# Kernel optimization log

Hardware: AMD Instinct MI355X
Metric: run time of the kernel (lower is better)

Reference implementation:

```python
import jax, jax.numpy as jnp
import numpy as np

H = 24
HEAD_DIM = 128
EPS = 1e-6
IP_SCALE = 1.0

def _rms(x, w):
    return x * jax.lax.rsqrt(jnp.mean(x * x, axis=-1, keepdims=True) + EPS) * w

def _heads(x, B):
    # (B, S, H*D) -> (B, H, S, D)
    return x.reshape(B, x.shape[1], H, HEAD_DIM).transpose(0, 2, 1, 3)

def _merge(x):
    B, h, S, d = x.shape
    return x.transpose(0, 2, 1, 3).reshape(B, S, h * d)

def _sdpa(q, k, v):
    s = jnp.einsum('bhqd,bhkd->bhqk', q, k) * (1.0 / np.sqrt(HEAD_DIM))
    return jnp.einsum('bhqk,bhkd->bhqd', jax.nn.softmax(s, axis=-1), v)

def _rope(x, cos, sin):
    # Flux-style real rotary: interleaved pairs, out = x*cos + rot(x)*sin
    xr = x.reshape(x.shape[:-1] + (-1, 2))
    x1, x2 = xr[..., 0], xr[..., 1]
    xrot = jnp.stack([-x2, x1], axis=-1).reshape(x.shape)
    return x * cos + xrot * sin

def setup_inputs():
    key = jax.random.key(0)
    ks = jax.random.split(key, 24)
    B, S_img, L_txt, D, IP_DIM, N_IP = 1, 2048, 512, 3072, 2048, 1024
    S = S_img + L_txt
    def w(k, i, o):
        return jax.random.normal(k, (i, o), jnp.float32) * 0.02
    def b(k, o):
        return jax.random.normal(k, (o,), jnp.float32) * 0.01
    pos = jnp.arange(S, dtype=jnp.float32)
    freqs = 1.0 / (10000.0 ** (jnp.arange(0, HEAD_DIM, 2, dtype=jnp.float32) / HEAD_DIM))
    ang = pos[:, None] * freqs[None, :]
    cos = jnp.repeat(jnp.cos(ang), 2, axis=-1)  # (S, HEAD_DIM)
    sin = jnp.repeat(jnp.sin(ang), 2, axis=-1)
    return {
        'hidden_states': jax.random.normal(ks[0], (B, S_img, D), jnp.float32),
        'encoder_hidden_states': jax.random.normal(ks[1], (B, L_txt, D), jnp.float32),
        'ip_hidden_states': jax.random.normal(ks[2], (B, N_IP, IP_DIM), jnp.float32),
        'rot_cos': cos, 'rot_sin': sin,
        'Wq': w(ks[3], D, D), 'bq': b(ks[4], D),
        'Wk': w(ks[5], D, D), 'bk': b(ks[6], D),
        'Wv': w(ks[7], D, D), 'bv': b(ks[8], D),
        'norm_q_w': jnp.ones((HEAD_DIM,), jnp.float32),
        'norm_k_w': jnp.ones((HEAD_DIM,), jnp.float32),
        'aWq': w(ks[9], D, D), 'abq': b(ks[10], D),
        'aWk': w(ks[11], D, D), 'abk': b(ks[12], D),
        'aWv': w(ks[13], D, D), 'abv': b(ks[14], D),
        'norm_aq_w': jnp.ones((HEAD_DIM,), jnp.float32),
        'norm_ak_w': jnp.ones((HEAD_DIM,), jnp.float32),
        'Wk_ip': w(ks[15], IP_DIM, D), 'bk_ip': b(ks[16], D),
        'Wv_ip': w(ks[17], IP_DIM, D), 'bv_ip': b(ks[18], D),
        'norm_ipq_w': jnp.ones((HEAD_DIM,), jnp.float32),
        'norm_ipk_w': jnp.ones((HEAD_DIM,), jnp.float32),
        'Wo': w(ks[19], D, D), 'bo': b(ks[20], D),
        'Wao': w(ks[21], D, D), 'bao': b(ks[22], D),
    }

def reference(hidden_states, encoder_hidden_states, ip_hidden_states, rot_cos, rot_sin,
              Wq, bq, Wk, bk, Wv, bv, norm_q_w, norm_k_w,
              aWq, abq, aWk, abk, aWv, abv, norm_aq_w, norm_ak_w,
              Wk_ip, bk_ip, Wv_ip, bv_ip, norm_ipq_w, norm_ipk_w,
              Wo, bo, Wao, bao):
    B, S_img, D = hidden_states.shape
    L = encoder_hidden_states.shape[1]
    q = _heads(hidden_states @ Wq + bq, B)   # (B,H,S_img,d)
    k = _heads(hidden_states @ Wk + bk, B)
    v = _heads(hidden_states @ Wv + bv, B)
    # IP-adapter cross-attention: RMS-normed raw image query vs projected image tokens
    ip_q = _rms(q, norm_ipq_w)
    ip_k = _rms(_heads(ip_hidden_states @ Wk_ip + bk_ip, B), norm_ipk_w)
    ip_v = _heads(ip_hidden_states @ Wv_ip + bv_ip, B)
    ip_out = _merge(_sdpa(ip_q, ip_k, ip_v))  # (B, S_img, D)
    # main joint attention with per-head QK RMSNorm
    q = _rms(q, norm_q_w)
    k = _rms(k, norm_k_w)
    eq = _rms(_heads(encoder_hidden_states @ aWq + abq, B), norm_aq_w)
    ek = _rms(_heads(encoder_hidden_states @ aWk + abk, B), norm_ak_w)
    ev = _heads(encoder_hidden_states @ aWv + abv, B)
    q = jnp.concatenate([eq, q], axis=2)
    k = jnp.concatenate([ek, k], axis=2)
    v = jnp.concatenate([ev, v], axis=2)
    q = _rope(q, rot_cos, rot_sin)
    k = _rope(k, rot_cos, rot_sin)
    hs = _merge(_sdpa(q, k, v))  # (B, L+S_img, D)
    enc = hs[:, :L]
    img = hs[:, L:] + IP_SCALE * ip_out
    img = img @ Wo + bo
    enc = enc @ Wao + bao
    return (img, enc)
```

## Files before the change

kernel.cpp:

```cpp
#include <hip/hip_runtime.h>
#include <hip/hip_bf16.h>
#include <cmath>
#include <cstdint>

#define H_    24
#define HD_   128
#define D_    3072
#define SIMG_ 2048
#define LTXT_ 512
#define SALL_ 2560
#define NIP_  1024
#define IPD_  2048

using bf16 = __hip_bfloat16;
typedef __bf16 bf16x8 __attribute__((ext_vector_type(8)));
typedef float  f32x4  __attribute__((ext_vector_type(4)));
typedef short  short8 __attribute__((ext_vector_type(8)));

#define QSCALE_ 0.12751741f

#define SWZ_BLOCK(bx, by)                                              \
  {                                                                    \
    int _gx = gridDim.x;                                               \
    int _hw = blockIdx.x + blockIdx.y * _gx;                           \
    int _n  = _gx * gridDim.y;                                         \
    int _lid = (_hw & 7) * (_n >> 3) + (_hw >> 3);                     \
    bx = _lid % _gx;                                                   \
    by = _lid / _gx;                                                   \
  }

__device__ __forceinline__ unsigned short f2bf(float f) {
  unsigned int u = __float_as_uint(f);
  unsigned int r = (u + 0x7fffu + ((u >> 16) & 1u)) >> 16;
  return (unsigned short)r;
}
__device__ __forceinline__ float bf2f(unsigned short u) {
  return __uint_as_float(((unsigned int)u) << 16);
}

__device__ __forceinline__ void gload16(const void* g, void* l) {
  __builtin_amdgcn_global_load_lds(
      (const __attribute__((address_space(1))) unsigned*)g,
      (__attribute__((address_space(3))) unsigned*)l, 16, 0, 0);
}

__global__ void cast_kernel(const float* __restrict__ x, unsigned short* __restrict__ y, int n4) {
  int i = blockIdx.x * blockDim.x + threadIdx.x;
  if (i >= n4) return;
  float4 v = reinterpret_cast<const float4*>(x)[i];
  ushort4 o = make_ushort4(f2bf(v.x), f2bf(v.y), f2bf(v.z), f2bf(v.w));
  reinterpret_cast<ushort4*>(y)[i] = o;
}

__global__ __launch_bounds__(512)
void transpose_cast3_kernel(const float* __restrict__ W0, const float* __restrict__ W1,
                            const float* __restrict__ W2, unsigned short* __restrict__ Wt,
                            int R, int C) {
  __shared__ float tile[32][69];
  const float* W = blockIdx.z == 0 ? W0 : (blockIdx.z == 1 ? W1 : W2);
  unsigned short* dst = Wt + (size_t)blockIdx.z * R * C;
  int bx = blockIdx.x * 64, by = blockIdx.y * 32;
  int tx = threadIdx.x, ty = threadIdx.y;
#pragma unroll
  for (int i = 0; i < 4; i++)
    tile[ty + 8 * i][tx] = W[(size_t)(by + ty + 8 * i) * C + bx + tx];
  __syncthreads();
  int t = ty * 64 + tx;
  int colr = t >> 3;
  int r0 = (t & 7) * 4;
  ushort4 o = make_ushort4(f2bf(tile[r0][colr]), f2bf(tile[r0 + 1][colr]),
                           f2bf(tile[r0 + 2][colr]), f2bf(tile[r0 + 3][colr]));
  *reinterpret_cast<ushort4*>(&dst[(size_t)(bx + colr) * R + by + r0]) = o;
}

__device__ __forceinline__ void gemm_core64(const bf16* __restrict__ Ab, const bf16* __restrict__ Bb,
                                            int K, bf16* Alds, bf16* Blds, int t,
                                            int wid, int l16, int lg, f32x4 (&acc)[2][8]) {
  char* AldsB = (char*)Alds + t * 16;
  char* BldsB = (char*)Blds + t * 16;
  for (int kt = 0; kt < K; kt += 64) {
    __syncthreads();
#pragma unroll
    for (int p = 0; p < 4; p++) {
      gload16(Ab + (size_t)(32 * p) * K + kt, AldsB + p * 4096);
      gload16(Bb + (size_t)(32 * p) * K + kt, BldsB + p * 4096);
    }
    __syncthreads();
#pragma unroll
    for (int kb = 0; kb < 2; kb++) {
      bf16x8 af[2], bfr[8];
#pragma unroll
      for (int mi = 0; mi < 2; mi++) {
        int r = wid * 32 + mi * 16 + l16;
        af[mi] = *reinterpret_cast<const bf16x8*>(
            (char*)Alds + r * 128 + ((lg * 16 + kb * 64) ^ ((r & 7) << 4)));
      }
#pragma unroll
      for (int ni = 0; ni < 8; ni++) {
        int r = ni * 16 + l16;
        bfr[ni] = *reinterpret_cast<const bf16x8*>(
            (char*)Blds + r * 128 + ((lg * 16 + kb * 64) ^ ((r & 7) << 4)));
      }
      __builtin_amdgcn_s_setprio(1);
#pragma unroll
      for (int mi = 0; mi < 2; mi++)
#pragma unroll
        for (int ni = 0; ni < 8; ni++)
          acc[mi][ni] = __builtin_amdgcn_mfma_f32_16x16x32_bf16(af[mi], bfr[ni], acc[mi][ni], 0, 0, 0);
      __builtin_amdgcn_s_setprio(0);
    }
  }
}

__global__ __launch_bounds__(256)
void gemm_proj_kernel(const bf16* __restrict__ A, const bf16* __restrict__ Wt,
                      int M, int K, int projmap,
                      const float* __restrict__ b0, const float* __restrict__ b1,
                      const float* __restrict__ b2,
                      const float* __restrict__ rcos, const float* __restrict__ rsin,
                      int pos_off, int tok_off, int Sout,
                      unsigned short* __restrict__ qa_p, const float* __restrict__ nq,
                      unsigned short* __restrict__ ipq_p, const float* __restrict__ nipq, int Sip,
                      unsigned short* __restrict__ ka_p, const float* __restrict__ nk,
                      unsigned short* __restrict__ va_p) {
  __shared__ __align__(16) bf16 Alds[128 * 64];
  __shared__ __align__(16) bf16 Blds[128 * 64];
  bf16* VtS = Alds;
  int t = threadIdx.x;
  int lane = t & 63, wid = t >> 6;
  int l16 = lane & 15, lg = lane >> 4;
  int bx, by;
  SWZ_BLOCK(bx, by);
  int bm = bx * 128;
  int proj = by / 24, head = by % 24;
  int code = (projmap >> (proj * 4)) & 15;
  int arow = t >> 3;
  int aseg = (t & 7) ^ (arow & 7);

  f32x4 acc[2][8];
#pragma unroll
  for (int i = 0; i < 2; i++)
#pragma unroll
    for (int j = 0; j < 8; j++) { acc[i][j][0]=0.f; acc[i][j][1]=0.f; acc[i][j][2]=0.f; acc[i][j][3]=0.f; }

  const bf16* Ab = A  + (size_t)(bm + arow) * K + aseg * 8;
  const bf16* Bb = Wt + (size_t)(by * 128 + arow) * K + aseg * 8;
  gemm_core64(Ab, Bb, K, Alds, Blds, t, wid, l16, lg, acc);

  const float* bias = proj == 0 ? b0 : (proj == 1 ? b1 : b2);
  int bcol = head * 128;

  if (code == 2) {
#pragma unroll
    for (int half = 0; half < 2; half++) {
      __syncthreads();
#pragma unroll
      for (int mi = 0; mi < 2; mi++)
#pragma unroll
        for (int j = 0; j < 4; j++) {
          int tok = wid * 32 + mi * 16 + lg * 4 + j;
#pragma unroll
          for (int ni = 0; ni < 4; ni++) {
            int col = l16 + 16 * ni;
            float val = acc[mi][ni + 4 * half][j] + bias[bcol + col + 64 * half];
            unsigned short uv = f2bf(val);
            VtS[col * 128 + (tok ^ ((col & 15) << 3))] = *(bf16*)&uv;
          }
        }
      __syncthreads();
      int colr = t >> 2;
      int tokbase = (t & 3) * 32;
#pragma unroll
      for (int it = 0; it < 4; it++) {
        int tok0 = tokbase + it * 8;
        short8 vv = *reinterpret_cast<const short8*>(&VtS[colr * 128 + (tok0 ^ ((colr & 15) << 3))]);
        *reinterpret_cast<short8*>(
            &va_p[((size_t)head * HD_ + 64 * half + colr) * Sout + tok_off + bm + tok0]) = vv;
      }
    }
    return;
  }

#pragma unroll
  for (int mi = 0; mi < 2; mi++) {
#pragma unroll
    for (int j = 0; j < 4; j++) {
      int rloc = wid * 32 + mi * 16 + lg * 4 + j;
      int row  = bm + rloc;
      float v[8];
#pragma unroll
      for (int ni = 0; ni < 8; ni++)
        v[ni] = acc[mi][ni][j] + bias[bcol + l16 + 16 * ni];

      float ss = 0.f;
#pragma unroll
      for (int ni = 0; ni < 8; ni++) ss += v[ni] * v[ni];
#pragma unroll
      for (int off = 1; off < 16; off <<= 1) ss += __shfl_xor(ss, off);
      float rr = rsqrtf(ss * (1.f / 128.f) + 1e-6f);

      auto emit = [&](unsigned short* outp, const float* nw, int rope, int scale,
                      int toff, int So) {
        float y[8];
#pragma unroll
        for (int ni = 0; ni < 8; ni++) {
          int col = l16 + 16 * ni;
          y[ni] = v[ni] * rr * nw[col];
        }
        if (rope) {
#pragma unroll
          for (int ni = 0; ni < 8; ni++) {
            int col = l16 + 16 * ni;
            float c  = rcos[(size_t)(pos_off + row) * HD_ + col];
            float sn = rsin[(size_t)(pos_off + row) * HD_ + col];
            float partner = __shfl_xor(y[ni], 1);
            y[ni] = y[ni] * c + ((col & 1) ? partner : -partner) * sn;
          }
        }
        if (scale) {
#pragma unroll
          for (int ni = 0; ni < 8; ni++) y[ni] *= QSCALE_;
        }
#pragma unroll
        for (int ni = 0; ni < 8; ni++) {
          int col = l16 + 16 * ni;
          outp[((size_t)head * So + toff + row) * HD_ + col] = f2bf(y[ni]);
        }
      };

      if (code == 0) {
        emit(qa_p, nq, 1, 1, tok_off, Sout);
        if (ipq_p) emit(ipq_p, nipq, 0, 1, 0, Sip);
      } else if (code == 1) {
        emit(ka_p, nk, 1, 0, tok_off, Sout);
      } else {
        emit(ka_p, nk, 0, 0, tok_off, Sout);
      }
    }
  }
}

__global__ __launch_bounds__(256)
void gemm_out2_kernel(const bf16* __restrict__ A_img, const bf16* __restrict__ A_enc,
                      const bf16* __restrict__ Wt,
                      const float* __restrict__ bo, const float* __restrict__ bao,
                      float* __restrict__ C_img, float* __restrict__ C_enc) {
  __shared__ __align__(16) bf16 Alds[128 * 64];
  __shared__ __align__(16) bf16 Blds[128 * 64];
  int t = threadIdx.x;
  int lane = t & 63, wid = t >> 6;
  int l16 = lane & 15, lg = lane >> 4;
  int bx, byn;
  SWZ_BLOCK(bx, byn);
  int is_enc = bx >= 16;
  const bf16* A = is_enc ? A_enc : A_img;
  const bf16* W = Wt + (is_enc ? (size_t)D_ * D_ : 0);
  const float* bias = is_enc ? bao : bo;
  float* C = is_enc ? C_enc : C_img;
  int bm = (is_enc ? bx - 16 : bx) * 128;
  int bn = byn * 128;
  int arow = t >> 3;
  int aseg = (t & 7) ^ (arow & 7);
  const int K = D_;

  f32x4 acc[2][8];
#pragma unroll
  for (int i = 0; i < 2; i++)
#pragma unroll
    for (int j = 0; j < 8; j++) { acc[i][j][0]=0.f; acc[i][j][1]=0.f; acc[i][j][2]=0.f; acc[i][j][3]=0.f; }

  const bf16* Ab = A + (size_t)(bm + arow) * K + aseg * 8;
  const bf16* Bb = W + (size_t)(bn + arow) * K + aseg * 8;
  gemm_core64(Ab, Bb, K, Alds, Blds, t, wid, l16, lg, acc);

#pragma unroll
  for (int mi = 0; mi < 2; mi++)
#pragma unroll
    for (int j = 0; j < 4; j++) {
      int row = bm + wid * 32 + mi * 16 + lg * 4 + j;
#pragma unroll
      for (int ni = 0; ni < 8; ni++)
        C[(size_t)row * D_ + bn + l16 + 16 * ni] = acc[mi][ni][j] + bias[bn + l16 + 16 * ni];
    }
}

__global__ __launch_bounds__(256)
void attn_kernel(const bf16* __restrict__ Q1, const bf16* __restrict__ K1,
                 const bf16* __restrict__ Vt1, unsigned short* __restrict__ O1,
                 int Sq1, int Skv1, int nx1,
                 const bf16* __restrict__ Q2, const bf16* __restrict__ K2,
                 const bf16* __restrict__ Vt2, unsigned short* __restrict__ O2,
                 int Sq2, int Skv2) {
  __shared__ __align__(16) bf16 Kl[64 * 128];
  __shared__ __align__(16) bf16 Vl[128 * 64];
  int t = threadIdx.x, lane = t & 63, wid = t >> 6;
  int l16 = lane & 15, lg = lane >> 4;
  int bx, h;
  SWZ_BLOCK(bx, h);
  int is2 = bx >= nx1;
  const bf16* Q  = is2 ? Q2  : Q1;
  const bf16* K  = is2 ? K2  : K1;
  const bf16* Vt = is2 ? Vt2 : Vt1;
  unsigned short* O = is2 ? O2 : O1;
  int Sq  = is2 ? Sq2  : Sq1;
  int Skv = is2 ? Skv2 : Skv1;
  int qb = (is2 ? bx - nx1 : bx) * 128 + wid * 32;

  const bf16* Qh  = Q  + (size_t)h * Sq * HD_;
  const bf16* Kh  = K  + (size_t)h * Skv * HD_;
  const bf16* Vth = Vt + (size_t)h * HD_ * Skv;

  bf16x8 qf[2][4];
#pragma unroll
  for (int m = 0; m < 2; m++)
#pragma unroll
    for (int kb = 0; kb < 4; kb++)
      qf[m][kb] = *reinterpret_cast<const bf16x8*>(
          &Qh[(size_t)(qb + m * 16 + l16) * HD_ + lg * 8 + kb * 32]);

  f32x4 acc[2][8];
#pragma unroll
  for (int m = 0; m < 2; m++)
#pragma unroll
    for (int cb = 0; cb < 8; cb++) { acc[m][cb][0]=0.f; acc[m][cb][1]=0.f; acc[m][cb][2]=0.f; acc[m][cb][3]=0.f; }
  float l_r[2] = {0.f, 0.f};

  int ksrow = t >> 4, kscol = t & 15;
  int vsrow = t >> 3, vscol = t & 7;

  for (int kt = 0; kt < Skv; kt += 64) {
    __syncthreads();
#pragma unroll
    for (int p = 0; p < 4; p++) {
      int r = p * 16 + ksrow;
      short8 kv = *reinterpret_cast<const short8*>(&Kh[(size_t)(kt + r) * HD_ + kscol * 8]);
      *reinterpret_cast<short8*>((char*)Kl + r * 256 + ((kscol * 16) ^ ((r & 7) << 4))) = kv;
    }
#pragma unroll
    for (int p = 0; p < 4; p++) {
      int d = p * 32 + vsrow;
      short8 vv = *reinterpret_cast<const short8*>(&Vth[(size_t)d * Skv + kt + vscol * 8]);
      *reinterpret_cast<short8*>((char*)Vl + d * 128 + ((vscol * 16) ^ ((d & 7) << 4))) = vv;
    }
    __syncthreads();

    f32x4 sc[2][4];
#pragma unroll
    for (int m = 0; m < 2; m++)
#pragma unroll
      for (int nb = 0; nb < 4; nb++) { sc[m][nb][0]=0.f; sc[m][nb][1]=0.f; sc[m][nb][2]=0.f; sc[m][nb][3]=0.f; }
    __builtin_amdgcn_s_setprio(1);
#pragma unroll
    for (int kb = 0; kb < 4; kb++) {
#pragma unroll
      for (int nb = 0; nb < 4; nb++) {
        int r = nb * 16 + l16;
        bf16x8 kf = *reinterpret_cast<const bf16x8*>(
            (char*)Kl + r * 256 + ((lg * 16 + kb * 64) ^ ((r & 7) << 4)));
        sc[0][nb] = __builtin_amdgcn_mfma_f32_16x16x32_bf16(kf, qf[0][kb], sc[0][nb], 0, 0, 0);
        sc[1][nb] = __builtin_amdgcn_mfma_f32_16x16x32_bf16(kf, qf[1][kb], sc[1][nb], 0, 0, 0);
      }
    }
    __builtin_amdgcn_s_setprio(0);
    __syncthreads();

#pragma unroll
    for (int m = 0; m < 2; m++) {
      float part = 0.f;
#pragma unroll
      for (int nb = 0; nb < 4; nb++)
#pragma unroll
        for (int j = 0; j < 4; j++) {
          float p = exp2f(sc[m][nb][j]);
          sc[m][nb][j] = p;
          part += p;
        }
      l_r[m] += part;
      char* Pb = (char*)Kl + (wid * 2 + m) * 2048 + l16 * 128;
#pragma unroll
      for (int nb = 0; nb < 4; nb++) {
#pragma unroll
        for (int w = 0; w < 2; w++) {
          unsigned int pk;
          asm("v_cvt_pk_bf16_f32 %0, %1, %2"
              : "=v"(pk) : "v"(sc[m][nb][2 * w]), "v"(sc[m][nb][2 * w + 1]));
          int colb = nb * 32 + lg * 8 + w * 4;
          *(unsigned int*)(Pb + (colb ^ ((l16 & 7) << 4))) = pk;
        }
      }
    }
    asm volatile("s_waitcnt lgkmcnt(0)" ::: "memory");

#pragma unroll
    for (int kb2 = 0; kb2 < 2; kb2++) {
      bf16x8 pa[2];
#pragma unroll
      for (int m = 0; m < 2; m++)
        pa[m] = *reinterpret_cast<const bf16x8*>(
            (char*)Kl + (wid * 2 + m) * 2048 + l16 * 128 + ((lg * 16 + kb2 * 64) ^ ((l16 & 7) << 4)));
      __builtin_amdgcn_s_setprio(1);
#pragma unroll
      for (int cb = 0; cb < 8; cb++) {
        int d = cb * 16 + l16;
        bf16x8 vf = *reinterpret_cast<const bf16x8*>(
            (char*)Vl + d * 128 + ((lg * 16 + kb2 * 64) ^ ((d & 7) << 4)));
        acc[0][cb] = __builtin_amdgcn_mfma_f32_16x16x32_bf16(pa[0], vf, acc[0][cb], 0, 0, 0);
        acc[1][cb] = __builtin_amdgcn_mfma_f32_16x16x32_bf16(pa[1], vf, acc[1][cb], 0, 0, 0);
      }
      __builtin_amdgcn_s_setprio(0);
    }
  }

#pragma unroll
  for (int m = 0; m < 2; m++) {
    l_r[m] += __shfl_xor(l_r[m], 16);
    l_r[m] += __shfl_xor(l_r[m], 32);
  }

#pragma unroll
  for (int m = 0; m < 2; m++) {
    float inv[4];
#pragma unroll
    for (int j = 0; j < 4; j++) inv[j] = 1.0f / __shfl(l_r[m], lg * 4 + j);
#pragma unroll
    for (int cb = 0; cb < 8; cb++) {
      int col = h * HD_ + l16 + 16 * cb;
#pragma unroll
      for (int j = 0; j < 4; j++) {
        int row = qb + m * 16 + lg * 4 + j;
        O[(size_t)row * (H_ * HD_) + col] = f2bf(acc[m][cb][j] * inv[j]);
      }
    }
  }
}

__global__ void combine_kernel(const unsigned short* __restrict__ attn,
                               const unsigned short* __restrict__ ipo,
                               unsigned short* __restrict__ img_in) {
  size_t i = ((size_t)blockIdx.x * blockDim.x + threadIdx.x) * 8;
  if (i >= (size_t)SIMG_ * D_) return;
  short8 a = *reinterpret_cast<const short8*>(attn + (size_t)LTXT_ * D_ + i);
  short8 b = *reinterpret_cast<const short8*>(ipo + i);
  short8 o;
#pragma unroll
  for (int j = 0; j < 8; j++)
    o[j] = (short)f2bf(bf2f((unsigned short)a[j]) + bf2f((unsigned short)b[j]));
  *reinterpret_cast<short8*>(img_in + i) = o;
}

extern "C" void kernel_launch(void* const* d_in, const int* in_sizes, int n_in,
                              void* d_out, int out_size, void* d_ws, size_t ws_size,
                              hipStream_t stream) {
  const float* hs   = (const float*)d_in[0];
  const float* ehs  = (const float*)d_in[1];
  const float* iphs = (const float*)d_in[2];
  const float* rcos = (const float*)d_in[3];
  const float* rsin = (const float*)d_in[4];
  const float* Wq   = (const float*)d_in[5];  const float* bq   = (const float*)d_in[6];
  const float* Wk   = (const float*)d_in[7];  const float* bk   = (const float*)d_in[8];
  const float* Wv   = (const float*)d_in[9];  const float* bv   = (const float*)d_in[10];
  const float* nqw  = (const float*)d_in[11]; const float* nkw  = (const float*)d_in[12];
  const float* aWq  = (const float*)d_in[13]; const float* abq  = (const float*)d_in[14];
  const float* aWk  = (const float*)d_in[15]; const float* abk  = (const float*)d_in[16];
  const float* aWv  = (const float*)d_in[17]; const float* abv  = (const float*)d_in[18];
  const float* naqw = (const float*)d_in[19]; const float* nakw = (const float*)d_in[20];
  const float* Wkip = (const float*)d_in[21]; const float* bkip = (const float*)d_in[22];
  const float* Wvip = (const float*)d_in[23]; const float* bvip = (const float*)d_in[24];
  const float* nipqw= (const float*)d_in[25]; const float* nipkw= (const float*)d_in[26];
  const float* Wo   = (const float*)d_in[27]; const float* bo   = (const float*)d_in[28];
  const float* Wao  = (const float*)d_in[29]; const float* bao  = (const float*)d_in[30];
  float* out_img = (float*)d_out;
  float* out_enc = out_img + (size_t)SIMG_ * D_;

  char* ws = (char*)d_ws;
  bf16*  Wt      = (bf16*)(ws + 0);
  unsigned short* attn_bf   = (unsigned short*)(ws + 37748736);
  bf16*  qa      = (bf16*)(ws + 56623104);
  bf16*  ka      = (bf16*)(ws + 72351744);
  bf16*  vaT     = (bf16*)(ws + 88080384);
  bf16*  ipq_bf  = (bf16*)(ws + 103809024);
  bf16*  ipk_bf  = (bf16*)(ws + 116391936);
  bf16*  ipvT   = (bf16*)(ws + 122683392);
  bf16*  act_bf  = (bf16*)(ws + 128974848);
  unsigned short* ip_out_bf = (unsigned short*)act_bf;
  bf16*  img_in  = (bf16*)qa;
  if (ws_size < 141557760) return;

  dim3 tb(64, 8);

  cast_kernel<<<SIMG_ * D_ / 4 / 256, 256, 0, stream>>>(hs, (unsigned short*)act_bf, SIMG_ * D_ / 4);
  transpose_cast3_kernel<<<dim3(48, 96, 3), tb, 0, stream>>>(Wq, Wk, Wv, (unsigned short*)Wt, D_, D_);
  gemm_proj_kernel<<<dim3(16, 72), 256, 0, stream>>>(act_bf, Wt, SIMG_, D_, 0x210,
      bq, bk, bv, rcos, rsin, LTXT_, LTXT_, SALL_,
      (unsigned short*)qa, nqw, (unsigned short*)ipq_bf, nipqw, SIMG_,
      (unsigned short*)ka, nkw, (unsigned short*)vaT);

  cast_kernel<<<LTXT_ * D_ / 4 / 256, 256, 0, stream>>>(ehs, (unsigned short*)act_bf, LTXT_ * D_ / 4);
  transpose_cast3_kernel<<<dim3(48, 96, 3), tb, 0, stream>>>(aWq, aWk, aWv, (unsigned short*)Wt, D_, D_);
  gemm_proj_kernel<<<dim3(4, 72), 256, 0, stream>>>(act_bf, Wt, LTXT_, D_, 0x210,
      abq, abk, abv, rcos, rsin, 0, 0, SALL_,
      (unsigned short*)qa, naqw, nullptr, nipqw, SIMG_,
      (unsigned short*)ka, nakw, (unsigned short*)vaT);

  cast_kernel<<<NIP_ * IPD_ / 4 / 256, 256, 0, stream>>>(iphs, (unsigned short*)act_bf, NIP_ * IPD_ / 4);
  transpose_cast3_kernel<<<dim3(48, 64, 2), tb, 0, stream>>>(Wkip, Wvip, Wvip, (unsigned short*)Wt, IPD_, D_);
  gemm_proj_kernel<<<dim3(8, 48), 256, 0, stream>>>(act_bf, Wt, NIP_, IPD_, 0x23,
      bkip, bvip, bvip, nullptr, nullptr, 0, 0, NIP_,
      nullptr, nullptr, nullptr, nullptr, 0,
      (unsigned short*)ipk_bf, nipkw, (unsigned short*)ipvT);

  transpose_cast3_kernel<<<dim3(48, 96, 2), tb, 0, stream>>>(Wo, Wao, Wao, (unsigned short*)Wt, D_, D_);

  attn_kernel<<<dim3(SALL_ / 128 + SIMG_ / 128, H_), 256, 0, stream>>>(
      qa, ka, vaT, attn_bf, SALL_, SALL_, SALL_ / 128,
      ipq_bf, ipk_bf, ipvT, ip_out_bf, SIMG_, NIP_);

  combine_kernel<<<SIMG_ * D_ / 8 / 256, 256, 0, stream>>>(attn_bf, ip_out_bf, (unsigned short*)img_in);

  gemm_out2_kernel<<<dim3(20, 24), 256, 0, stream>>>(img_in, (const bf16*)attn_bf, Wt,
                                                     bo, bao, out_img, out_enc);
}
```

Measured before the change: 670.7 us.

## Permute head-dim layout for packed Q/K stores, async LDS loads in attention, wider transpose

Switches the projection epilogue to a permuted head-dimension layout so each lane writes 8 contiguous bf16 values with packed conversions and a single vector store. The V transpose and the attention output column mapping are adjusted to match the permutation. The attention K/V tile loads now go straight to LDS via global_load_lds with an XOR swizzle on the source address instead of staging through registers. The weight transpose-cast kernel now uses 64x64 tiles with float4 reads and 16-byte writes. The permutation must stay consistent across all producers and consumers, and the RoPE partner shuffle may become wrong under the new layout.

```diff
diff --git a/kernel.cpp b/kernel.cpp
--- a/kernel.cpp
+++ b/kernel.cpp
@@ -16,6 +16,7 @@
 typedef __bf16 bf16x8 __attribute__((ext_vector_type(8)));
 typedef float  f32x4  __attribute__((ext_vector_type(4)));
 typedef short  short8 __attribute__((ext_vector_type(8)));
+typedef unsigned int uint4v __attribute__((ext_vector_type(4)));
 
 #define QSCALE_ 0.12751741f
 
@@ -37,12 +38,18 @@
 __device__ __forceinline__ float bf2f(unsigned short u) {
   return __uint_as_float(((unsigned int)u) << 16);
 }
+__device__ __forceinline__ unsigned int cvtpk(float lo, float hi) {
+  unsigned int pk;
+  asm("v_cvt_pk_bf16_f32 %0, %1, %2" : "=v"(pk) : "v"(lo), "v"(hi));
+  return pk;
+}
 
 __device__ __forceinline__ void gload16(const void* g, void* l) {
   __builtin_amdgcn_global_load_lds(
       (const __attribute__((address_space(1))) unsigned*)g,
       (__attribute__((address_space(3))) unsigned*)l, 16, 0, 0);
 }
+
 
 __global__ void cast_kernel(const float* __restrict__ x, unsigned short* __restrict__ y, int n4) {
   int i = blockIdx.x * blockDim.x + threadIdx.x;
@@ -56,21 +63,25 @@
 void transpose_cast3_kernel(const float* __restrict__ W0, const float* __restrict__ W1,
                             const float* __restrict__ W2, unsigned short* __restrict__ Wt,
                             int R, int C) {
-  __shared__ float tile[32][69];
+  __shared__ float tile[64][69];
   const float* W = blockIdx.z == 0 ? W0 : (blockIdx.z == 1 ? W1 : W2);
   unsigned short* dst = Wt + (size_t)blockIdx.z * R * C;
-  int bx = blockIdx.x * 64, by = blockIdx.y * 32;
+  int bx = blockIdx.x * 64, by = blockIdx.y * 64;
   int tx = threadIdx.x, ty = threadIdx.y;
 #pragma unroll
-  for (int i = 0; i < 4; i++)
-    tile[ty + 8 * i][tx] = W[(size_t)(by + ty + 8 * i) * C + bx + tx];
+  for (int i = 0; i < 2; i++) {
+    int r = ty + 32 * i;
+    float4 v = *reinterpret_cast<const float4*>(&W[(size_t)(by + r) * C + bx + tx * 4]);
+    tile[r][tx * 4 + 0] = v.x; tile[r][tx * 4 + 1] = v.y;
+    tile[r][tx * 4 + 2] = v.z; tile[r][tx * 4 + 3] = v.w;
+  }
   __syncthreads();
-  int t = ty * 64 + tx;
-  int colr = t >> 3;
-  int r0 = (t & 7) * 4;
-  ushort4 o = make_ushort4(f2bf(tile[r0][colr]), f2bf(tile[r0 + 1][colr]),
-                           f2bf(tile[r0 + 2][colr]), f2bf(tile[r0 + 3][colr]));
-  *reinterpret_cast<ushort4*>(&dst[(size_t)(bx + colr) * R + by + r0]) = o;
+  int tid = ty * 16 + tx;
+  int c = tid >> 3, r0 = (tid & 7) * 8;
+  short8 o;
+#pragma unroll
+  for (int j = 0; j < 8; j++) o[j] = (short)f2bf(tile[r0 + j][c]);
+  *reinterpret_cast<short8*>(&dst[(size_t)(bx + c) * R + by + r0]) = o;
 }
 
 __device__ __forceinline__ void gemm_core64(const bf16* __restrict__ Ab, const bf16* __restrict__ Bb,
@@ -161,21 +172,22 @@
           int tok = wid * 32 + mi * 16 + lg * 4 + j;
 #pragma unroll
           for (int ni = 0; ni < 4; ni++) {
-            int col = l16 + 16 * ni;
-            float val = acc[mi][ni + 4 * half][j] + bias[bcol + col + 64 * half];
+            int rc = l16 * 4 + ni;
+            float val = acc[mi][ni + 4 * half][j] + bias[bcol + l16 + 16 * (ni + 4 * half)];
             unsigned short uv = f2bf(val);
-            VtS[col * 128 + (tok ^ ((col & 15) << 3))] = *(bf16*)&uv;
+            VtS[rc * 128 + (tok ^ ((rc & 15) << 3))] = *(bf16*)&uv;
           }
         }
       __syncthreads();
-      int colr = t >> 2;
+      int rc = t >> 2;
       int tokbase = (t & 3) * 32;
+      int s = (rc >> 2) * 8 + (rc & 3) + 4 * half;
 #pragma unroll
       for (int it = 0; it < 4; it++) {
         int tok0 = tokbase + it * 8;
-        short8 vv = *reinterpret_cast<const short8*>(&VtS[colr * 128 + (tok0 ^ ((colr & 15) << 3))]);
+        short8 vv = *reinterpret_cast<const short8*>(&VtS[rc * 128 + (tok0 ^ ((rc & 15) << 3))]);
         *reinterpret_cast<short8*>(
-            &va_p[((size_t)head * HD_ + 64 * half + colr) * Sout + tok_off + bm + tok0]) = vv;
+            &va_p[((size_t)head * HD_ + s) * Sout + tok_off + bm + tok0]) = vv;
       }
     }
     return;
@@ -221,11 +233,10 @@
 #pragma unroll
           for (int ni = 0; ni < 8; ni++) y[ni] *= QSCALE_;
         }
-#pragma unroll
-        for (int ni = 0; ni < 8; ni++) {
-          int col = l16 + 16 * ni;
-          outp[((size_t)head * So + toff + row) * HD_ + col] = f2bf(y[ni]);
-        }
+        uint4v pk;
+        pk[0] = cvtpk(y[0], y[1]); pk[1] = cvtpk(y[2], y[3]);
+        pk[2] = cvtpk(y[4], y[5]); pk[3] = cvtpk(y[6], y[7]);
+        *reinterpret_cast<uint4v*>(&outp[((size_t)head * So + toff + row) * HD_ + l16 * 8]) = pk;
       };
 
       if (code == 0) {
@@ -325,22 +336,21 @@
     for (int cb = 0; cb < 8; cb++) { acc[m][cb][0]=0.f; acc[m][cb][1]=0.f; acc[m][cb][2]=0.f; acc[m][cb][3]=0.f; }
   float l_r[2] = {0.f, 0.f};
 
-  int ksrow = t >> 4, kscol = t & 15;
-  int vsrow = t >> 3, vscol = t & 7;
+  int krow = t >> 4;
+  int vrow = t >> 3;
+  char* KlB = (char*)Kl + t * 16;
+  char* VlB = (char*)Vl + t * 16;
 
   for (int kt = 0; kt < Skv; kt += 64) {
     __syncthreads();
 #pragma unroll
     for (int p = 0; p < 4; p++) {
-      int r = p * 16 + ksrow;
-      short8 kv = *reinterpret_cast<const short8*>(&Kh[(size_t)(kt + r) * HD_ + kscol * 8]);
-      *reinterpret_cast<short8*>((char*)Kl + r * 256 + ((kscol * 16) ^ ((r & 7) << 4))) = kv;
-    }
-#pragma unroll
-    for (int p = 0; p < 4; p++) {
-      int d = p * 32 + vsrow;
-      short8 vv = *reinterpret_cast<const short8*>(&Vth[(size_t)d * Skv + kt + vscol * 8]);
-      *reinterpret_cast<short8*>((char*)Vl + d * 128 + ((vscol * 16) ^ ((d & 7) << 4))) = vv;
+      int rk = p * 16 + krow;
+      int sk = (t & 15) ^ (rk & 7);
+      gload16(Kh + (size_t)(kt + rk) * HD_ + sk * 8, KlB + p * 4096);
+      int rv = p * 32 + vrow;
+      int sv = (t & 7) ^ (rv & 7);
+      gload16(Vth + (size_t)rv * Skv + kt + sv * 8, VlB + p * 4096);
     }
     __syncthreads();
 
@@ -381,9 +391,7 @@
       for (int nb = 0; nb < 4; nb++) {
 #pragma unroll
         for (int w = 0; w < 2; w++) {
-          unsigned int pk;
-          asm("v_cvt_pk_bf16_f32 %0, %1, %2"
-              : "=v"(pk) : "v"(sc[m][nb][2 * w]), "v"(sc[m][nb][2 * w + 1]));
+          unsigned int pk = cvtpk(sc[m][nb][2 * w], sc[m][nb][2 * w + 1]);
           int colb = nb * 32 + lg * 8 + w * 4;
           *(unsigned int*)(Pb + (colb ^ ((l16 & 7) << 4))) = pk;
         }
@@ -424,7 +432,7 @@
     for (int j = 0; j < 4; j++) inv[j] = 1.0f / __shfl(l_r[m], lg * 4 + j);
 #pragma unroll
     for (int cb = 0; cb < 8; cb++) {
-      int col = h * HD_ + l16 + 16 * cb;
+      int col = h * HD_ + (l16 & 7) * 16 + cb * 2 + (l16 >> 3);
 #pragma unroll
       for (int j = 0; j < 4; j++) {
         int row = qb + m * 16 + lg * 4 + j;
@@ -486,30 +494,30 @@
   bf16*  img_in  = (bf16*)qa;
   if (ws_size < 141557760) return;
 
-  dim3 tb(64, 8);
+  dim3 tb2(16, 32);
 
   cast_kernel<<<SIMG_ * D_ / 4 / 256, 256, 0, stream>>>(hs, (unsigned short*)act_bf, SIMG_ * D_ / 4);
-  transpose_cast3_kernel<<<dim3(48, 96, 3), tb, 0, stream>>>(Wq, Wk, Wv, (unsigned short*)Wt, D_, D_);
+  transpose_cast3_kernel<<<dim3(48, 48, 3), tb2, 0, stream>>>(Wq, Wk, Wv, (unsigned short*)Wt, D_, D_);
   gemm_proj_kernel<<<dim3(16, 72), 256, 0, stream>>>(act_bf, Wt, SIMG_, D_, 0x210,
       bq, bk, bv, rcos, rsin, LTXT_, LTXT_, SALL_,
       (unsigned short*)qa, nqw, (unsigned short*)ipq_bf, nipqw, SIMG_,
       (unsigned short*)ka, nkw, (unsigned short*)vaT);
 
   cast_kernel<<<LTXT_ * D_ / 4 / 256, 256, 0, stream>>>(ehs, (unsigned short*)act_bf, LTXT_ * D_ / 4);
-  transpose_cast3_kernel<<<dim3(48, 96, 3), tb, 0, stream>>>(aWq, aWk, aWv, (unsigned short*)Wt, D_, D_);
+  transpose_cast3_kernel<<<dim3(48, 48, 3), tb2, 0, stream>>>(aWq, aWk, aWv, (unsigned short*)Wt, D_, D_);
   gemm_proj_kernel<<<dim3(4, 72), 256, 0, stream>>>(act_bf, Wt, LTXT_, D_, 0x210,
       abq, abk, abv, rcos, rsin, 0, 0, SALL_,
       (unsigned short*)qa, naqw, nullptr, nipqw, SIMG_,
       (unsigned short*)ka, nakw, (unsigned short*)vaT);
 
   cast_kernel<<<NIP_ * IPD_ / 4 / 256, 256, 0, stream>>>(iphs, (unsigned short*)act_bf, NIP_ * IPD_ / 4);
-  transpose_cast3_kernel<<<dim3(48, 64, 2), tb, 0, stream>>>(Wkip, Wvip, Wvip, (unsigned short*)Wt, IPD_, D_);
+  transpose_cast3_kernel<<<dim3(48, 32, 2), tb2, 0, stream>>>(Wkip, Wvip, Wvip, (unsigned short*)Wt, IPD_, D_);
   gemm_proj_kernel<<<dim3(8, 48), 256, 0, stream>>>(act_bf, Wt, NIP_, IPD_, 0x23,
       bkip, bvip, bvip, nullptr, nullptr, 0, 0, NIP_,
       nullptr, nullptr, nullptr, nullptr, 0,
       (unsigned short*)ipk_bf, nipkw, (unsigned short*)ipvT);
 
-  transpose_cast3_kernel<<<dim3(48, 96, 2), tb, 0, stream>>>(Wo, Wao, Wao, (unsigned short*)Wt, D_, D_);
+  transpose_cast3_kernel<<<dim3(48, 48, 2), tb2, 0, stream>>>(Wo, Wao, Wao, (unsigned short*)Wt, D_, D_);
 
   attn_kernel<<<dim3(SALL_ / 128 + SIMG_ / 128, H_), 256, 0, stream>>>(
       qa, ka, vaT, attn_bf, SALL_, SALL_, SALL_ / 128,
```

New measurement: 669.1 us. Within noise of the previous version (-0.2%).
